# Performance work log

Hardware: AMD Instinct MI355X
Metric: run time of the kernel (lower is better)

## Reference

```python
import jax, jax.numpy as jnp
import numpy as np

EPS = 1e-5

def maxpool2(x):
    # 2x2 max pool, stride 2, NCHW
    B, C, H, W = x.shape
    return x.reshape(B, C, H // 2, 2, W // 2, 2).max(axis=(3, 5))

def conv1x1(x, w, b):
    # x: [B,C,H,W], w: [O,C], b: [O]
    return jnp.einsum('bchw,oc->bohw', x, w) + b[None, :, None, None]

def setup_inputs() -> dict:
    key = jax.random.key(0)
    ks = jax.random.split(key, 12)
    B, C, IC, H, W = 8, 256, 128, 128, 128
    s = 0.05
    return {
        'rgb': jax.random.normal(ks[0], (B, C, H, W), jnp.float32),
        'event': jax.random.normal(ks[1], (B, C, H, W), jnp.float32),
        'g_w': jax.random.normal(ks[2], (IC, C), jnp.float32) * s,
        'g_b': jax.random.normal(ks[3], (IC,), jnp.float32) * s,
        'theta_w': jax.random.normal(ks[4], (IC, C), jnp.float32) * s,
        'theta_b': jax.random.normal(ks[5], (IC,), jnp.float32) * s,
        'phi_w': jax.random.normal(ks[6], (IC, C), jnp.float32) * s,
        'phi_b': jax.random.normal(ks[7], (IC,), jnp.float32) * s,
        'W_w': jax.random.normal(ks[8], (C, IC), jnp.float32) * s,
        'W_b': jax.random.normal(ks[9], (C,), jnp.float32) * s,
        'bn_gamma': jax.random.normal(ks[10], (C,), jnp.float32) * s + 1.0,
        'bn_beta': jax.random.normal(ks[11], (C,), jnp.float32) * s,
    }

def reference(rgb, event, g_w, g_b, theta_w, theta_b, phi_w, phi_b, W_w, W_b, bn_gamma, bn_beta):
    B = rgb.shape[0]
    IC = g_w.shape[0]
    # initial shared 2x2 max pool on both modalities
    rgb_p = maxpool2(rgb)      # [B,C,h2,w2]
    ev_p = maxpool2(event)
    h2, w2 = rgb_p.shape[2], rgb_p.shape[3]
    # projections; g and phi have an extra sub_sample pool
    g_x = maxpool2(conv1x1(ev_p, g_w, g_b)).reshape(B, IC, -1)      # [B,IC,Nkv]
    g_x = jnp.swapaxes(g_x, 1, 2)                                    # [B,Nkv,IC]
    theta_x = conv1x1(rgb_p, theta_w, theta_b).reshape(B, IC, -1)    # [B,IC,Nq]
    theta_x = jnp.swapaxes(theta_x, 1, 2)                            # [B,Nq,IC]
    phi_x = maxpool2(conv1x1(ev_p, phi_w, phi_b)).reshape(B, IC, -1) # [B,IC,Nkv]
    # full attention: scores -> softmax -> value matmul
    f = jnp.einsum('bqc,bck->bqk', theta_x, phi_x)                   # [B,Nq,Nkv]
    f_div_C = jax.nn.softmax(f, axis=-1)
    y = jnp.einsum('bqk,bkc->bqc', f_div_C, g_x)                     # [B,Nq,IC]
    y = jnp.swapaxes(y, 1, 2).reshape(B, IC, h2, w2)
    # output 1x1 conv + BatchNorm (training-mode batch stats, biased var)
    W_y = conv1x1(y, W_w, W_b)                                       # [B,C,h2,w2]
    mean = W_y.mean(axis=(0, 2, 3), keepdims=True)
    var = W_y.var(axis=(0, 2, 3), keepdims=True)
    W_y = (W_y - mean) * jax.lax.rsqrt(var + EPS)
    W_y = W_y * bn_gamma[None, :, None, None] + bn_beta[None, :, None, None]
    z = W_y + rgb_p
    z = jnp.repeat(jnp.repeat(z, 2, axis=2), 2, axis=3)
    return z
```

## Files before the change

kernel.cpp:

```cpp
#include <hip/hip_runtime.h>
#include <stdint.h>


typedef unsigned short u16;
typedef short bf16x8 __attribute__((ext_vector_type(8)));
typedef float f32x4 __attribute__((ext_vector_type(4)));

#define MFMA16(a, b, c) __builtin_amdgcn_mfma_f32_16x16x32_bf16(a, b, c, 0, 0, 0)

__device__ __forceinline__ u16 f2bf(float x) {
    union { float f; unsigned int u; } v; v.f = x;
    unsigned int u = v.u;
    unsigned int r = u + 0x7fffu + ((u >> 16) & 1u);
    return (u16)(r >> 16);
}
__device__ __forceinline__ float bf2f(u16 h) {
    union { unsigned int u; float f; } v; v.u = ((unsigned int)h) << 16;
    return v.f;
}

__global__ void zero_kernel(float* __restrict__ p, int n) {
    int i = blockIdx.x * 256 + threadIdx.x;
    if (i < n) p[i] = 0.0f;
}

__global__ __launch_bounds__(256) void pool_transpose_kernel(
    const float* __restrict__ x, u16* __restrict__ ohi, u16* __restrict__ olo) {
    __shared__ float tile[64][65];
    int bx = blockIdx.x;
    int ct = bx & 3, h2 = (bx >> 2) & 63, b = bx >> 8;
    int tid = threadIdx.x;
    int col = tid & 127;
    int chalf = tid >> 7;

    long base_in = (((long)b * 256 + ct * 64) * 128 + 2 * h2) * 128;
#pragma unroll 4
    for (int i = 0; i < 32; i++) {
        int c_l = i * 2 + chalf;
        const float* p = x + base_in + (long)c_l * 16384;
        float m = fmaxf(p[col], p[128 + col]);
        float o = __shfl_xor(m, 1);
        m = fmaxf(m, o);
        if ((col & 1) == 0) tile[col >> 1][c_l] = m;
    }
    __syncthreads();
    long obase = ((long)b * 4096 + h2 * 64) * 256 + ct * 64;
#pragma unroll 4
    for (int i = 0; i < 8; i++) {
        int idx = i * 512 + tid * 2;
        int w2 = idx >> 6, c_l = idx & 63;
        float v0 = tile[w2][c_l], v1 = tile[w2][c_l + 1];
        u16 h0 = f2bf(v0), h1 = f2bf(v1);
        ushort2 hh; hh.x = h0; hh.y = h1;
        ushort2 ll; ll.x = f2bf(v0 - bf2f(h0)); ll.y = f2bf(v1 - bf2f(h1));
        long oi = obase + (long)w2 * 256 + c_l;
        *(ushort2*)&ohi[oi] = hh;
        *(ushort2*)&olo[oi] = ll;
    }
}

__global__ void wsplit_kernel(const float* __restrict__ tw, const float* __restrict__ pw,
                              const float* __restrict__ gw, const float* __restrict__ ww,
                              u16* __restrict__ planes) {
    int idx = blockIdx.x * 256 + threadIdx.x;
    int m = idx >> 15, e = idx & 32767;
    const float* src = (m == 0) ? tw : (m == 1) ? pw : (m == 2) ? gw : ww;
    float v = src[e];
    u16 h = f2bf(v);
    planes[m * 65536 + e] = h;
    planes[m * 65536 + 32768 + e] = f2bf(v - bf2f(h));
}

template <int K, int O, bool SPLIT, int OMODE, int RG>
__global__ __launch_bounds__(256) void conv1x1_kernel(
    const u16* __restrict__ Ahi, const u16* __restrict__ Alo,
    const u16* __restrict__ Whi, const u16* __restrict__ Wlo,
    const float* __restrict__ bias,
    u16* __restrict__ out_hi, u16* __restrict__ out_lo, float* __restrict__ out_f) {
    constexpr int NT = O / 16;
    int tid = threadIdx.x;
    int wave = tid >> 6, lane = tid & 63, quad = lane >> 4, l16 = lane & 15;
    long mbase = (long)blockIdx.x * (64 * RG) + wave * (16 * RG);

    f32x4 acc[RG][NT];
#pragma unroll
    for (int rg = 0; rg < RG; rg++)
#pragma unroll
        for (int nt = 0; nt < NT; nt++)
#pragma unroll
            for (int r = 0; r < 4; r++) acc[rg][nt][r] = 0.0f;

#pragma unroll
    for (int kc = 0; kc < K / 32; kc++) {
        bf16x8 ah[RG], al[RG];
#pragma unroll
        for (int rg = 0; rg < RG; rg++) {
            long arow = mbase + rg * 16 + l16;
            ah[rg] = *(const bf16x8*)&Ahi[arow * K + kc * 32 + quad * 8];
            if (SPLIT) al[rg] = *(const bf16x8*)&Alo[arow * K + kc * 32 + quad * 8];
        }
#pragma unroll
        for (int nt = 0; nt < NT; nt++) {
            long wrow = (long)(nt * 16 + l16) * K + kc * 32 + quad * 8;
            bf16x8 bh = *(const bf16x8*)&Whi[wrow];
            bf16x8 bl;
            if (SPLIT) bl = *(const bf16x8*)&Wlo[wrow];
#pragma unroll
            for (int rg = 0; rg < RG; rg++) {
                acc[rg][nt] = MFMA16(ah[rg], bh, acc[rg][nt]);
                if (SPLIT) {
                    acc[rg][nt] = MFMA16(ah[rg], bl, acc[rg][nt]);
                    acc[rg][nt] = MFMA16(al[rg], bh, acc[rg][nt]);
                }
            }
        }
    }

#pragma unroll
    for (int rg = 0; rg < RG; rg++)
#pragma unroll
        for (int nt = 0; nt < NT; nt++) {
            int colo = nt * 16 + l16;
            float bv = bias[colo];
#pragma unroll
            for (int r = 0; r < 4; r++) {
                long row = mbase + rg * 16 + quad * 4 + r;
                float v = acc[rg][nt][r] + bv;
                long idx = row * O + colo;
                if (OMODE == 2) {
                    out_f[idx] = v;
                } else if (OMODE == 0) {
                    out_hi[idx] = f2bf(v);
                } else {
                    u16 h = f2bf(v);
                    out_hi[idx] = h;
                    out_lo[idx] = f2bf(v - bf2f(h));
                }
            }
        }
}

__global__ __launch_bounds__(256) void conv_phig_kernel(
    const u16* __restrict__ Ahi, const u16* __restrict__ Alo,
    const u16* __restrict__ Wph, const u16* __restrict__ Wpl,
    const u16* __restrict__ Wgh,
    const float* __restrict__ phi_b, const float* __restrict__ g_b,
    u16* __restrict__ phi_hi, u16* __restrict__ phi_lo, u16* __restrict__ gout) {
    int tid = threadIdx.x;
    int wave = tid >> 6, lane = tid & 63, quad = lane >> 4, l16 = lane & 15;
    long mbase = (long)blockIdx.x * 128 + wave * 32;

    f32x4 ap[2][8], ag[2][8];
#pragma unroll
    for (int rg = 0; rg < 2; rg++)
#pragma unroll
        for (int nt = 0; nt < 8; nt++)
#pragma unroll
            for (int r = 0; r < 4; r++) { ap[rg][nt][r] = 0.0f; ag[rg][nt][r] = 0.0f; }

#pragma unroll
    for (int kc = 0; kc < 8; kc++) {
        bf16x8 ah[2], al[2];
#pragma unroll
        for (int rg = 0; rg < 2; rg++) {
            long arow = mbase + rg * 16 + l16;
            ah[rg] = *(const bf16x8*)&Ahi[arow * 256 + kc * 32 + quad * 8];
            al[rg] = *(const bf16x8*)&Alo[arow * 256 + kc * 32 + quad * 8];
        }
#pragma unroll
        for (int nt = 0; nt < 8; nt++) {
            long wrow = (long)(nt * 16 + l16) * 256 + kc * 32 + quad * 8;
            bf16x8 bph = *(const bf16x8*)&Wph[wrow];
            bf16x8 bpl = *(const bf16x8*)&Wpl[wrow];
            bf16x8 bgh = *(const bf16x8*)&Wgh[wrow];
#pragma unroll
            for (int rg = 0; rg < 2; rg++) {
                ap[rg][nt] = MFMA16(ah[rg], bph, ap[rg][nt]);
                ap[rg][nt] = MFMA16(ah[rg], bpl, ap[rg][nt]);
                ap[rg][nt] = MFMA16(al[rg], bph, ap[rg][nt]);
                ag[rg][nt] = MFMA16(ah[rg], bgh, ag[rg][nt]);
            }
        }
    }

#pragma unroll
    for (int rg = 0; rg < 2; rg++)
#pragma unroll
        for (int nt = 0; nt < 8; nt++) {
            int colo = nt * 16 + l16;
            float pb = phi_b[colo], gb = g_b[colo];
#pragma unroll
            for (int r = 0; r < 4; r++) {
                long row = mbase + rg * 16 + quad * 4 + r;
                long idx = row * 128 + colo;
                float vp = ap[rg][nt][r] + pb;
                u16 h = f2bf(vp);
                phi_hi[idx] = h;
                phi_lo[idx] = f2bf(vp - bf2f(h));
                gout[idx] = f2bf(ag[rg][nt][r] + gb);
            }
        }
}

__global__ __launch_bounds__(256) void pool_phiK_kernel(
    const u16* __restrict__ fhi, const u16* __restrict__ flo,
    u16* __restrict__ khi, u16* __restrict__ klo) {
    int idx = blockIdx.x * 256 + threadIdx.x;
    int c8 = (idx & 15) * 8;
    int kv = (idx >> 4) & 1023;
    int b = idx >> 14;
    int h4 = kv >> 5, w4 = kv & 31;
    long p00 = ((long)b * 4096 + (2 * h4) * 64 + 2 * w4) * 128 + c8;
    bf16x8 h0 = *(const bf16x8*)&fhi[p00];
    bf16x8 h1 = *(const bf16x8*)&fhi[p00 + 128];
    bf16x8 h2 = *(const bf16x8*)&fhi[p00 + 8192];
    bf16x8 h3 = *(const bf16x8*)&fhi[p00 + 8320];
    bf16x8 l0 = *(const bf16x8*)&flo[p00];
    bf16x8 l1 = *(const bf16x8*)&flo[p00 + 128];
    bf16x8 l2 = *(const bf16x8*)&flo[p00 + 8192];
    bf16x8 l3 = *(const bf16x8*)&flo[p00 + 8320];
    bf16x8 oh, ol;
#pragma unroll
    for (int e = 0; e < 8; e++) {
        float v = fmaxf(fmaxf(bf2f((u16)h0[e]) + bf2f((u16)l0[e]),
                              bf2f((u16)h1[e]) + bf2f((u16)l1[e])),
                        fmaxf(bf2f((u16)h2[e]) + bf2f((u16)l2[e]),
                              bf2f((u16)h3[e]) + bf2f((u16)l3[e])));
        u16 h = f2bf(v);
        oh[e] = (short)h;
        ol[e] = (short)f2bf(v - bf2f(h));
    }
    long oi = ((long)b * 1024 + kv) * 128 + c8;
    *(bf16x8*)&khi[oi] = oh;
    *(bf16x8*)&klo[oi] = ol;
}

__global__ __launch_bounds__(256) void pool_gVt_kernel(
    const u16* __restrict__ g, u16* __restrict__ vt) {
    __shared__ u16 t[64][65];
    int bx = blockIdx.x;
    int ct = bx & 1, kvt = (bx >> 1) & 15, b = bx >> 5;
    int tid = threadIdx.x;
#pragma unroll 4
    for (int i = 0; i < 16; i++) {
        int idx = i * 256 + tid;
        int kv_l = idx >> 6, c_l = idx & 63;
        int kv = kvt * 64 + kv_l;
        int h4 = kv >> 5, w4 = kv & 31;
        long p00 = ((long)b * 4096 + (2 * h4) * 64 + 2 * w4) * 128 + ct * 64 + c_l;
        float v = fmaxf(fmaxf(bf2f(g[p00]), bf2f(g[p00 + 128])),
                        fmaxf(bf2f(g[p00 + 8192]), bf2f(g[p00 + 8192 + 128])));
        t[c_l][kv_l] = f2bf(v);
    }
    __syncthreads();
    long ob = ((long)b * 128 + ct * 64) * 1024 + kvt * 64;
#pragma unroll 4
    for (int i = 0; i < 16; i++) {
        int idx = i * 256 + tid;
        int c_l = idx >> 6, kv_l = idx & 63;
        vt[ob + (long)c_l * 1024 + kv_l] = t[c_l][kv_l];
    }
}

__global__ __launch_bounds__(512, 4) void attn_kernel(
    const u16* __restrict__ th, const u16* __restrict__ tl,
    const u16* __restrict__ khi, const u16* __restrict__ klo,
    const u16* __restrict__ vt, u16* __restrict__ y) {
    __shared__ u16 Kh[2][32][136];
    __shared__ u16 Kl[2][32][136];
    __shared__ u16 Vt[2][128][40];
    __shared__ u16 Pl[8][16][40];

    int bx = blockIdx.x;
    int b = bx & 7, qt = bx >> 3;
    int tid = threadIdx.x;
    int w = tid >> 6, g = w >> 2, wsub = w & 3;
    int lane = tid & 63, quad = lane >> 4, l16 = lane & 15;
    int qbase = qt * 64 + wsub * 16;

    bf16x8 qh[4], ql[4];
    long tb = ((long)b * 4096 + qbase + l16) * 128;
#pragma unroll
    for (int kc = 0; kc < 4; kc++) {
        qh[kc] = *(const bf16x8*)&th[tb + kc * 32 + quad * 8];
        ql[kc] = *(const bf16x8*)&tl[tb + kc * 32 + quad * 8];
    }

    f32x4 o[8];
#pragma unroll
    for (int t2 = 0; t2 < 8; t2++)
#pragma unroll
        for (int r = 0; r < 4; r++) o[t2][r] = 0.0f;
    float lp[4] = {0.0f, 0.0f, 0.0f, 0.0f};

#pragma unroll 1
    for (int it = 0; it < 16; it++) {
        __syncthreads();
#pragma unroll
        for (int j = 0; j < 2; j++) {
            int c0 = j * 512 + tid;
            int row = (c0 >> 4) & 31, ko = (c0 & 15) * 8;
            long src = ((long)b * 1024 + j * 512 + it * 32 + row) * 128 + ko;
            *(uint4*)&Kh[j][row][ko] = *(const uint4*)&khi[src];
            *(uint4*)&Kl[j][row][ko] = *(const uint4*)&klo[src];
        }
#pragma unroll
        for (int j = 0; j < 2; j++) {
            int c0 = j * 512 + tid;
            int crow = (c0 >> 2) & 127, ko = (c0 & 3) * 8;
            long src = ((long)b * 128 + crow) * 1024 + j * 512 + it * 32 + ko;
            *(uint4*)&Vt[j][crow][ko] = *(const uint4*)&vt[src];
        }
        __syncthreads();

        f32x4 s[2];
#pragma unroll
        for (int nt = 0; nt < 2; nt++)
#pragma unroll
            for (int r = 0; r < 4; r++) s[nt][r] = 0.0f;
#pragma unroll
        for (int kc = 0; kc < 4; kc++) {
#pragma unroll
            for (int nt = 0; nt < 2; nt++) {
                bf16x8 bh = *(const bf16x8*)&Kh[g][nt * 16 + l16][kc * 32 + quad * 8];
                bf16x8 bl = *(const bf16x8*)&Kl[g][nt * 16 + l16][kc * 32 + quad * 8];
                s[nt] = MFMA16(qh[kc], bh, s[nt]);
                s[nt] = MFMA16(qh[kc], bl, s[nt]);
                s[nt] = MFMA16(ql[kc], bh, s[nt]);
            }
        }

#pragma unroll
        for (int nt = 0; nt < 2; nt++)
#pragma unroll
            for (int r = 0; r < 4; r++) {
                float p = __expf(s[nt][r]);
                lp[r] += p;
                Pl[w][quad * 4 + r][nt * 16 + l16] = f2bf(p);
            }

        bf16x8 pa = *(const bf16x8*)&Pl[w][l16][quad * 8];
#pragma unroll
        for (int t2 = 0; t2 < 8; t2++) {
            bf16x8 vb = *(const bf16x8*)&Vt[g][t2 * 16 + l16][quad * 8];
            o[t2] = MFMA16(pa, vb, o[t2]);
        }
    }

#pragma unroll
    for (int r = 0; r < 4; r++)
#pragma unroll
        for (int off = 1; off < 16; off <<= 1) lp[r] += __shfl_xor(lp[r], off);

    __syncthreads();
    float* Ob = (float*)&Kh[0][0][0];
    float* Lb = (float*)&Vt[0][0][0];
    if (g == 1) {
#pragma unroll
        for (int t2 = 0; t2 < 8; t2++)
#pragma unroll
            for (int r = 0; r < 4; r++)
                Ob[(wsub * 16 + quad * 4 + r) * 132 + t2 * 16 + l16] = o[t2][r];
        if (l16 == 0)
#pragma unroll
            for (int r = 0; r < 4; r++) Lb[wsub * 16 + quad * 4 + r] = lp[r];
    }
    __syncthreads();
    if (g == 0) {
#pragma unroll
        for (int r = 0; r < 4; r++) {
            int lrow = wsub * 16 + quad * 4 + r;
            float inv = 1.0f / (lp[r] + Lb[lrow]);
            long row = (long)b * 4096 + qbase + quad * 4 + r;
#pragma unroll
            for (int t2 = 0; t2 < 8; t2++) {
                float ov = o[t2][r] + Ob[lrow * 132 + t2 * 16 + l16];
                y[row * 128 + t2 * 16 + l16] = f2bf(ov * inv);
            }
        }
    }
}

__global__ __launch_bounds__(256) void bnstat_kernel(const float* __restrict__ wy,
                                                     float* __restrict__ acc) {
    int c = threadIdx.x;
    long r0 = (long)blockIdx.x * 32;
    float s = 0.0f, q = 0.0f;
#pragma unroll 4
    for (int i = 0; i < 32; i++) {
        float v = wy[(r0 + i) * 256 + c];
        s += v;
        q += v * v;
    }
    atomicAdd(&acc[c], s);
    atomicAdd(&acc[256 + c], q);
}

__global__ __launch_bounds__(256) void final_kernel(
    const float* __restrict__ wy, const u16* __restrict__ rgbhi,
    const float* __restrict__ acc, const float* __restrict__ gamma,
    const float* __restrict__ beta, float* __restrict__ out) {
    __shared__ float z[16][257];
    int bx = blockIdx.x;
    int wt = bx & 3, h2 = (bx >> 2) & 63, b = bx >> 8;
    int c = threadIdx.x;

    float mean = acc[c] * (1.0f / 32768.0f);
    float var = acc[256 + c] * (1.0f / 32768.0f) - mean * mean;
    float rstd = rsqrtf(var + 1e-5f);
    float gm = gamma[c] * rstd;
    float bt = beta[c] - mean * gm;

    long pbase = (long)b * 4096 + h2 * 64 + wt * 16;
#pragma unroll 4
    for (int i = 0; i < 16; i++) {
        long pi = (pbase + i) * 256 + c;
        z[i][c] = wy[pi] * gm + bt + bf2f(rgbhi[pi]);
    }
    __syncthreads();
    int tid = threadIdx.x;
#pragma unroll 4
    for (int pass = 0; pass < 64; pass++) {
        int cc = pass * 4 + (tid >> 6);
        int r = (tid >> 5) & 1, wc = tid & 31;
        float v = z[wc >> 1][cc];
        out[(((long)b * 256 + cc) * 128 + 2 * h2 + r) * 128 + wt * 32 + wc] = v;
    }
}

extern "C" void kernel_launch(void* const* d_in, const int* in_sizes, int n_in,
                              void* d_out, int out_size, void* d_ws, size_t ws_size,
                              hipStream_t stream) {
    const float* rgb     = (const float*)d_in[0];
    const float* event_  = (const float*)d_in[1];
    const float* g_w     = (const float*)d_in[2];
    const float* g_b     = (const float*)d_in[3];
    const float* theta_w = (const float*)d_in[4];
    const float* theta_b = (const float*)d_in[5];
    const float* phi_w   = (const float*)d_in[6];
    const float* phi_b   = (const float*)d_in[7];
    const float* W_w     = (const float*)d_in[8];
    const float* W_b     = (const float*)d_in[9];
    const float* gamma   = (const float*)d_in[10];
    const float* beta    = (const float*)d_in[11];

    char* ws = (char*)d_ws;
    u16* rgbpt_hi = (u16*)(ws + 0);
    u16* rgbpt_lo = (u16*)(ws + 16777216);
    u16* evpt_hi  = (u16*)(ws + 33554432);
    u16* evpt_lo  = (u16*)(ws + 50331648);
    u16* theta_hi = (u16*)(ws + 67108864);
    u16* theta_lo = (u16*)(ws + 75497472);
    u16* phiF_hi  = (u16*)(ws + 83886080);
    u16* phiF_lo  = (u16*)(ws + 92274688);
    u16* g_full   = (u16*)(ws + 100663296);
    u16* phiK_hi  = (u16*)(ws + 109051904);
    u16* phiK_lo  = (u16*)(ws + 111149056);
    u16* gVt      = (u16*)(ws + 113246208);
    u16* y        = phiF_hi;
    float* Wy     = (float*)(ws + 16777216);
    u16* wplanes  = (u16*)(ws + 115343360);
    float* acc    = (float*)(ws + 115867648);

    zero_kernel<<<2, 256, 0, stream>>>(acc, 512);
    pool_transpose_kernel<<<2048, 256, 0, stream>>>(rgb, rgbpt_hi, rgbpt_lo);
    pool_transpose_kernel<<<2048, 256, 0, stream>>>(event_, evpt_hi, evpt_lo);
    wsplit_kernel<<<512, 256, 0, stream>>>(theta_w, phi_w, g_w, W_w, wplanes);

    conv1x1_kernel<256, 128, true, 1, 2><<<256, 256, 0, stream>>>(
        rgbpt_hi, rgbpt_lo, wplanes + 0, wplanes + 32768, theta_b,
        theta_hi, theta_lo, nullptr);
    conv_phig_kernel<<<256, 256, 0, stream>>>(
        evpt_hi, evpt_lo, wplanes + 65536, wplanes + 98304, wplanes + 131072,
        phi_b, g_b, phiF_hi, phiF_lo, g_full);

    pool_phiK_kernel<<<512, 256, 0, stream>>>(phiF_hi, phiF_lo, phiK_hi, phiK_lo);
    pool_gVt_kernel<<<256, 256, 0, stream>>>(g_full, gVt);

    attn_kernel<<<512, 512, 0, stream>>>(theta_hi, theta_lo, phiK_hi, phiK_lo, gVt, y);

    conv1x1_kernel<128, 256, false, 2, 1><<<512, 256, 0, stream>>>(
        y, nullptr, wplanes + 196608, nullptr, W_b, nullptr, nullptr, Wy);

    bnstat_kernel<<<1024, 256, 0, stream>>>(Wy, acc);
    final_kernel<<<2048, 256, 0, stream>>>(Wy, rgbpt_hi, acc, gamma, beta, (float*)d_out);
}
```

Baseline: 559.5 us.

## Fuse max-pool/transpose into projection convs and BN stats into output conv

The pooled bf16 hi/lo planes are no longer written to and re-read from global memory. Instead each block pools one row of the fp32 input into a swizzled shared-memory tile, splits it to hi/lo bf16 in registers and runs the theta or phi+g 1x1 conv MFMAs directly. The rgb pass also writes only the bf16 hi pooled plane needed by the final residual add. The output W conv now reduces per-channel sum and sum-of-squares in-block and atomically accumulates them, which removes the separate BN-stat pass over Wy. In exchange the kernels use 64KB of shared memory per block, which limits occupancy, and each block covers only 64 rows with one row group per wave.

```diff
diff --git a/kernel.cpp b/kernel.cpp
--- a/kernel.cpp
+++ b/kernel.cpp
@@ -22,41 +22,6 @@
 __global__ void zero_kernel(float* __restrict__ p, int n) {
     int i = blockIdx.x * 256 + threadIdx.x;
     if (i < n) p[i] = 0.0f;
-}
-
-__global__ __launch_bounds__(256) void pool_transpose_kernel(
-    const float* __restrict__ x, u16* __restrict__ ohi, u16* __restrict__ olo) {
-    __shared__ float tile[64][65];
-    int bx = blockIdx.x;
-    int ct = bx & 3, h2 = (bx >> 2) & 63, b = bx >> 8;
-    int tid = threadIdx.x;
-    int col = tid & 127;
-    int chalf = tid >> 7;
-
-    long base_in = (((long)b * 256 + ct * 64) * 128 + 2 * h2) * 128;
-#pragma unroll 4
-    for (int i = 0; i < 32; i++) {
-        int c_l = i * 2 + chalf;
-        const float* p = x + base_in + (long)c_l * 16384;
-        float m = fmaxf(p[col], p[128 + col]);
-        float o = __shfl_xor(m, 1);
-        m = fmaxf(m, o);
-        if ((col & 1) == 0) tile[col >> 1][c_l] = m;
-    }
-    __syncthreads();
-    long obase = ((long)b * 4096 + h2 * 64) * 256 + ct * 64;
-#pragma unroll 4
-    for (int i = 0; i < 8; i++) {
-        int idx = i * 512 + tid * 2;
-        int w2 = idx >> 6, c_l = idx & 63;
-        float v0 = tile[w2][c_l], v1 = tile[w2][c_l + 1];
-        u16 h0 = f2bf(v0), h1 = f2bf(v1);
-        ushort2 hh; hh.x = h0; hh.y = h1;
-        ushort2 ll; ll.x = f2bf(v0 - bf2f(h0)); ll.y = f2bf(v1 - bf2f(h1));
-        long oi = obase + (long)w2 * 256 + c_l;
-        *(ushort2*)&ohi[oi] = hh;
-        *(ushort2*)&olo[oi] = ll;
-    }
 }
 
 __global__ void wsplit_kernel(const float* __restrict__ tw, const float* __restrict__ pw,
@@ -71,135 +36,109 @@
     planes[m * 65536 + 32768 + e] = f2bf(v - bf2f(h));
 }
 
-template <int K, int O, bool SPLIT, int OMODE, int RG>
-__global__ __launch_bounds__(256) void conv1x1_kernel(
-    const u16* __restrict__ Ahi, const u16* __restrict__ Alo,
-    const u16* __restrict__ Whi, const u16* __restrict__ Wlo,
-    const float* __restrict__ bias,
-    u16* __restrict__ out_hi, u16* __restrict__ out_lo, float* __restrict__ out_f) {
-    constexpr int NT = O / 16;
+template <bool GCONV, bool POOLOUT>
+__global__ __launch_bounds__(256) void fused_pool_conv_kernel(
+    const float* __restrict__ x,
+    const u16* __restrict__ W1h, const u16* __restrict__ W1l,
+    const float* __restrict__ b1,
+    const u16* __restrict__ W2h, const float* __restrict__ b2,
+    u16* __restrict__ o1_hi, u16* __restrict__ o1_lo, u16* __restrict__ o2,
+    u16* __restrict__ pool_hi) {
+    __shared__ float Pt[64 * 256];
+
+    int bx = blockIdx.x;
+    int b = bx >> 6, h2 = bx & 63;
     int tid = threadIdx.x;
+
+    long ibase = (long)b * 256 * 16384 + (long)(2 * h2) * 128;
+#pragma unroll 8
+    for (int i = 0; i < 32; i++) {
+        int u = i * 256 + tid;
+        int c = u >> 5, w4 = u & 31;
+        const float* p = &x[ibase + (long)c * 16384 + w4 * 4];
+        float4 r0 = *(const float4*)p;
+        float4 r1 = *(const float4*)(p + 128);
+        float p0 = fmaxf(fmaxf(r0.x, r0.y), fmaxf(r1.x, r1.y));
+        float p1 = fmaxf(fmaxf(r0.z, r0.w), fmaxf(r1.z, r1.w));
+        int row0 = 2 * w4, row1 = 2 * w4 + 1;
+        Pt[row0 * 256 + (((((c >> 2)) ^ (row0 & 31)) << 2) | (c & 3))] = p0;
+        Pt[row1 * 256 + (((((c >> 2)) ^ (row1 & 31)) << 2) | (c & 3))] = p1;
+    }
+    __syncthreads();
+
     int wave = tid >> 6, lane = tid & 63, quad = lane >> 4, l16 = lane & 15;
-    long mbase = (long)blockIdx.x * (64 * RG) + wave * (16 * RG);
-
-    f32x4 acc[RG][NT];
-#pragma unroll
-    for (int rg = 0; rg < RG; rg++)
-#pragma unroll
-        for (int nt = 0; nt < NT; nt++)
-#pragma unroll
-            for (int r = 0; r < 4; r++) acc[rg][nt][r] = 0.0f;
-
-#pragma unroll
-    for (int kc = 0; kc < K / 32; kc++) {
-        bf16x8 ah[RG], al[RG];
-#pragma unroll
-        for (int rg = 0; rg < RG; rg++) {
-            long arow = mbase + rg * 16 + l16;
-            ah[rg] = *(const bf16x8*)&Ahi[arow * K + kc * 32 + quad * 8];
-            if (SPLIT) al[rg] = *(const bf16x8*)&Alo[arow * K + kc * 32 + quad * 8];
-        }
-#pragma unroll
-        for (int nt = 0; nt < NT; nt++) {
-            long wrow = (long)(nt * 16 + l16) * K + kc * 32 + quad * 8;
-            bf16x8 bh = *(const bf16x8*)&Whi[wrow];
-            bf16x8 bl;
-            if (SPLIT) bl = *(const bf16x8*)&Wlo[wrow];
-#pragma unroll
-            for (int rg = 0; rg < RG; rg++) {
-                acc[rg][nt] = MFMA16(ah[rg], bh, acc[rg][nt]);
-                if (SPLIT) {
-                    acc[rg][nt] = MFMA16(ah[rg], bl, acc[rg][nt]);
-                    acc[rg][nt] = MFMA16(al[rg], bh, acc[rg][nt]);
-                }
-            }
-        }
-    }
-
-#pragma unroll
-    for (int rg = 0; rg < RG; rg++)
-#pragma unroll
-        for (int nt = 0; nt < NT; nt++) {
-            int colo = nt * 16 + l16;
-            float bv = bias[colo];
-#pragma unroll
-            for (int r = 0; r < 4; r++) {
-                long row = mbase + rg * 16 + quad * 4 + r;
-                float v = acc[rg][nt][r] + bv;
-                long idx = row * O + colo;
-                if (OMODE == 2) {
-                    out_f[idx] = v;
-                } else if (OMODE == 0) {
-                    out_hi[idx] = f2bf(v);
-                } else {
-                    u16 h = f2bf(v);
-                    out_hi[idx] = h;
-                    out_lo[idx] = f2bf(v - bf2f(h));
-                }
-            }
-        }
-}
-
-__global__ __launch_bounds__(256) void conv_phig_kernel(
-    const u16* __restrict__ Ahi, const u16* __restrict__ Alo,
-    const u16* __restrict__ Wph, const u16* __restrict__ Wpl,
-    const u16* __restrict__ Wgh,
-    const float* __restrict__ phi_b, const float* __restrict__ g_b,
-    u16* __restrict__ phi_hi, u16* __restrict__ phi_lo, u16* __restrict__ gout) {
-    int tid = threadIdx.x;
-    int wave = tid >> 6, lane = tid & 63, quad = lane >> 4, l16 = lane & 15;
-    long mbase = (long)blockIdx.x * 128 + wave * 32;
-
-    f32x4 ap[2][8], ag[2][8];
-#pragma unroll
-    for (int rg = 0; rg < 2; rg++)
-#pragma unroll
-        for (int nt = 0; nt < 8; nt++)
-#pragma unroll
-            for (int r = 0; r < 4; r++) { ap[rg][nt][r] = 0.0f; ag[rg][nt][r] = 0.0f; }
+    int arow = wave * 16 + l16;
+
+    f32x4 a1[8];
+    f32x4 a2[GCONV ? 8 : 1];
+#pragma unroll
+    for (int nt = 0; nt < 8; nt++) {
+#pragma unroll
+        for (int r = 0; r < 4; r++) a1[nt][r] = 0.0f;
+        if (GCONV)
+#pragma unroll
+            for (int r = 0; r < 4; r++) a2[nt][r] = 0.0f;
+    }
 
 #pragma unroll
     for (int kc = 0; kc < 8; kc++) {
-        bf16x8 ah[2], al[2];
-#pragma unroll
-        for (int rg = 0; rg < 2; rg++) {
-            long arow = mbase + rg * 16 + l16;
-            ah[rg] = *(const bf16x8*)&Ahi[arow * 256 + kc * 32 + quad * 8];
-            al[rg] = *(const bf16x8*)&Alo[arow * 256 + kc * 32 + quad * 8];
+        int g0 = kc * 8 + quad * 2;
+        float4 fA = *(const float4*)&Pt[arow * 256 + ((g0 ^ (arow & 31)) << 2)];
+        float4 fB = *(const float4*)&Pt[arow * 256 + (((g0 + 1) ^ (arow & 31)) << 2)];
+        float vv[8] = {fA.x, fA.y, fA.z, fA.w, fB.x, fB.y, fB.z, fB.w};
+        bf16x8 ah, al;
+#pragma unroll
+        for (int e = 0; e < 8; e++) {
+            u16 h = f2bf(vv[e]);
+            ah[e] = (short)h;
+            al[e] = (short)f2bf(vv[e] - bf2f(h));
         }
 #pragma unroll
         for (int nt = 0; nt < 8; nt++) {
             long wrow = (long)(nt * 16 + l16) * 256 + kc * 32 + quad * 8;
-            bf16x8 bph = *(const bf16x8*)&Wph[wrow];
-            bf16x8 bpl = *(const bf16x8*)&Wpl[wrow];
-            bf16x8 bgh = *(const bf16x8*)&Wgh[wrow];
-#pragma unroll
-            for (int rg = 0; rg < 2; rg++) {
-                ap[rg][nt] = MFMA16(ah[rg], bph, ap[rg][nt]);
-                ap[rg][nt] = MFMA16(ah[rg], bpl, ap[rg][nt]);
-                ap[rg][nt] = MFMA16(al[rg], bph, ap[rg][nt]);
-                ag[rg][nt] = MFMA16(ah[rg], bgh, ag[rg][nt]);
+            bf16x8 bh = *(const bf16x8*)&W1h[wrow];
+            bf16x8 bl = *(const bf16x8*)&W1l[wrow];
+            a1[nt] = MFMA16(ah, bh, a1[nt]);
+            a1[nt] = MFMA16(ah, bl, a1[nt]);
+            a1[nt] = MFMA16(al, bh, a1[nt]);
+            if (GCONV) {
+                bf16x8 bg = *(const bf16x8*)&W2h[wrow];
+                a2[nt] = MFMA16(ah, bg, a2[nt]);
             }
         }
     }
 
-#pragma unroll
-    for (int rg = 0; rg < 2; rg++)
-#pragma unroll
-        for (int nt = 0; nt < 8; nt++) {
-            int colo = nt * 16 + l16;
-            float pb = phi_b[colo], gb = g_b[colo];
-#pragma unroll
-            for (int r = 0; r < 4; r++) {
-                long row = mbase + rg * 16 + quad * 4 + r;
-                long idx = row * 128 + colo;
-                float vp = ap[rg][nt][r] + pb;
-                u16 h = f2bf(vp);
-                phi_hi[idx] = h;
-                phi_lo[idx] = f2bf(vp - bf2f(h));
-                gout[idx] = f2bf(ag[rg][nt][r] + gb);
-            }
-        }
+    long mbase = (long)b * 4096 + h2 * 64;
+#pragma unroll
+    for (int nt = 0; nt < 8; nt++) {
+        int colo = nt * 16 + l16;
+        float bv1 = b1[colo];
+        float bv2 = GCONV ? b2[colo] : 0.0f;
+#pragma unroll
+        for (int r = 0; r < 4; r++) {
+            long row = mbase + wave * 16 + quad * 4 + r;
+            long idx = row * 128 + colo;
+            float v = a1[nt][r] + bv1;
+            u16 h = f2bf(v);
+            o1_hi[idx] = h;
+            o1_lo[idx] = f2bf(v - bf2f(h));
+            if (GCONV) o2[idx] = f2bf(a2[nt][r] + bv2);
+        }
+    }
+
+    if (POOLOUT) {
+#pragma unroll 4
+        for (int i = 0; i < 32; i++) {
+            int r = i * 2 + (tid >> 7);
+            int c = (tid & 127) * 2;
+            int g = c >> 2;
+            float2 f = *(const float2*)&Pt[r * 256 + (((g ^ (r & 31)) << 2) | (c & 3))];
+            ushort2 hh;
+            hh.x = f2bf(f.x);
+            hh.y = f2bf(f.y);
+            *(ushort2*)&pool_hi[(mbase + r) * 256 + c] = hh;
+        }
+    }
 }
 
 __global__ __launch_bounds__(256) void pool_phiK_kernel(
@@ -381,19 +320,59 @@
     }
 }
 
-__global__ __launch_bounds__(256) void bnstat_kernel(const float* __restrict__ wy,
-                                                     float* __restrict__ acc) {
-    int c = threadIdx.x;
-    long r0 = (long)blockIdx.x * 32;
-    float s = 0.0f, q = 0.0f;
-#pragma unroll 4
-    for (int i = 0; i < 32; i++) {
-        float v = wy[(r0 + i) * 256 + c];
-        s += v;
-        q += v * v;
-    }
-    atomicAdd(&acc[c], s);
-    atomicAdd(&acc[256 + c], q);
+__global__ __launch_bounds__(256) void wconv_kernel(
+    const u16* __restrict__ A, const u16* __restrict__ Wh,
+    const float* __restrict__ bias, float* __restrict__ out_f,
+    float* __restrict__ acc_g) {
+    __shared__ float red[4][2][256];
+    int tid = threadIdx.x;
+    int wave = tid >> 6, lane = tid & 63, quad = lane >> 4, l16 = lane & 15;
+    long mbase = (long)blockIdx.x * 64 + wave * 16;
+
+    f32x4 acc[16];
+#pragma unroll
+    for (int nt = 0; nt < 16; nt++)
+#pragma unroll
+        for (int r = 0; r < 4; r++) acc[nt][r] = 0.0f;
+
+#pragma unroll
+    for (int kc = 0; kc < 4; kc++) {
+        bf16x8 ah = *(const bf16x8*)&A[(mbase + l16) * 128 + kc * 32 + quad * 8];
+#pragma unroll
+        for (int nt = 0; nt < 16; nt++) {
+            bf16x8 bh = *(const bf16x8*)&Wh[(long)(nt * 16 + l16) * 128 + kc * 32 + quad * 8];
+            acc[nt] = MFMA16(ah, bh, acc[nt]);
+        }
+    }
+
+#pragma unroll
+    for (int nt = 0; nt < 16; nt++) {
+        int colo = nt * 16 + l16;
+        float bv = bias[colo];
+        float vs = 0.0f, vq = 0.0f;
+#pragma unroll
+        for (int r = 0; r < 4; r++) {
+            long row = mbase + quad * 4 + r;
+            float v = acc[nt][r] + bv;
+            out_f[row * 256 + colo] = v;
+            vs += v;
+            vq += v * v;
+        }
+        vs += __shfl_xor(vs, 16); vs += __shfl_xor(vs, 32);
+        vq += __shfl_xor(vq, 16); vq += __shfl_xor(vq, 32);
+        if (quad == 0) {
+            red[wave][0][colo] = vs;
+            red[wave][1][colo] = vq;
+        }
+    }
+    __syncthreads();
+    if (tid < 256) {
+        int c = tid;
+        float s = red[0][0][c] + red[1][0][c] + red[2][0][c] + red[3][0][c];
+        float q = red[0][1][c] + red[1][1][c] + red[2][1][c] + red[3][1][c];
+        atomicAdd(&acc_g[c], s);
+        atomicAdd(&acc_g[256 + c], q);
+    }
 }
 
 __global__ __launch_bounds__(256) void final_kernel(
@@ -446,42 +425,35 @@
 
     char* ws = (char*)d_ws;
     u16* rgbpt_hi = (u16*)(ws + 0);
-    u16* rgbpt_lo = (u16*)(ws + 16777216);
-    u16* evpt_hi  = (u16*)(ws + 33554432);
-    u16* evpt_lo  = (u16*)(ws + 50331648);
-    u16* theta_hi = (u16*)(ws + 67108864);
-    u16* theta_lo = (u16*)(ws + 75497472);
-    u16* phiF_hi  = (u16*)(ws + 83886080);
-    u16* phiF_lo  = (u16*)(ws + 92274688);
-    u16* g_full   = (u16*)(ws + 100663296);
-    u16* phiK_hi  = (u16*)(ws + 109051904);
-    u16* phiK_lo  = (u16*)(ws + 111149056);
-    u16* gVt      = (u16*)(ws + 113246208);
-    u16* y        = phiF_hi;
-    float* Wy     = (float*)(ws + 16777216);
-    u16* wplanes  = (u16*)(ws + 115343360);
-    float* acc    = (float*)(ws + 115867648);
+    u16* theta_hi = (u16*)(ws + 16777216);
+    u16* theta_lo = (u16*)(ws + 25165824);
+    u16* phiF_hi  = (u16*)(ws + 33554432);
+    u16* phiF_lo  = (u16*)(ws + 41943040);
+    u16* g_full   = (u16*)(ws + 50331648);
+    u16* phiK_hi  = (u16*)(ws + 58720256);
+    u16* phiK_lo  = (u16*)(ws + 60817408);
+    u16* gVt      = (u16*)(ws + 62914560);
+    u16* y        = (u16*)(ws + 65011712);
+    float* Wy     = (float*)(ws + 73400320);
+    u16* wplanes  = (u16*)(ws + 106954752);
+    float* acc    = (float*)(ws + 107479040);
 
     zero_kernel<<<2, 256, 0, stream>>>(acc, 512);
-    pool_transpose_kernel<<<2048, 256, 0, stream>>>(rgb, rgbpt_hi, rgbpt_lo);
-    pool_transpose_kernel<<<2048, 256, 0, stream>>>(event_, evpt_hi, evpt_lo);
     wsplit_kernel<<<512, 256, 0, stream>>>(theta_w, phi_w, g_w, W_w, wplanes);
 
-    conv1x1_kernel<256, 128, true, 1, 2><<<256, 256, 0, stream>>>(
-        rgbpt_hi, rgbpt_lo, wplanes + 0, wplanes + 32768, theta_b,
-        theta_hi, theta_lo, nullptr);
-    conv_phig_kernel<<<256, 256, 0, stream>>>(
-        evpt_hi, evpt_lo, wplanes + 65536, wplanes + 98304, wplanes + 131072,
-        phi_b, g_b, phiF_hi, phiF_lo, g_full);
+    fused_pool_conv_kernel<false, true><<<512, 256, 0, stream>>>(
+        rgb, wplanes + 0, wplanes + 32768, theta_b,
+        nullptr, nullptr, theta_hi, theta_lo, nullptr, rgbpt_hi);
+    fused_pool_conv_kernel<true, false><<<512, 256, 0, stream>>>(
+        event_, wplanes + 65536, wplanes + 98304, phi_b,
+        wplanes + 131072, g_b, phiF_hi, phiF_lo, g_full, nullptr);
 
     pool_phiK_kernel<<<512, 256, 0, stream>>>(phiF_hi, phiF_lo, phiK_hi, phiK_lo);
     pool_gVt_kernel<<<256, 256, 0, stream>>>(g_full, gVt);
 
     attn_kernel<<<512, 512, 0, stream>>>(theta_hi, theta_lo, phiK_hi, phiK_lo, gVt, y);
 
-    conv1x1_kernel<128, 256, false, 2, 1><<<512, 256, 0, stream>>>(
-        y, nullptr, wplanes + 196608, nullptr, W_b, nullptr, nullptr, Wy);
-
-    bnstat_kernel<<<1024, 256, 0, stream>>>(Wy, acc);
+    wconv_kernel<<<512, 256, 0, stream>>>(y, wplanes + 196608, W_b, Wy, acc);
+
     final_kernel<<<2048, 256, 0, stream>>>(Wy, rgbpt_hi, acc, gamma, beta, (float*)d_out);
 }
```

Result: faster. 542.7 us (-3.0%).
